# Optimization experiments

Hardware: AMD Instinct MI355X
Metric: run time of the kernel (lower is better)

The kernel has to match this reference:

```python
import jax, jax.numpy as jnp
import numpy as np

B, L, C = 8, 2048, 512
CI = C // 2  # internal_units


def setup_inputs() -> dict:
    key = jax.random.key(0)
    ks = jax.random.split(key, 4)
    inputs = jax.random.normal(ks[0], (B, L, C), dtype=jnp.float32)
    # Conv1D kernel_size=1 == per-position linear; kernel_initializer='random_normal' (stddev 0.05)
    Wx = 0.05 * jax.random.normal(ks[1], (C, CI), dtype=jnp.float32)
    Wy = 0.05 * jax.random.normal(ks[2], (C, CI), dtype=jnp.float32)
    Wo = 0.05 * jax.random.normal(ks[3], (C, C), dtype=jnp.float32)
    bx = jnp.zeros((CI,), dtype=jnp.float32)
    by = jnp.zeros((CI,), dtype=jnp.float32)
    bo = jnp.zeros((C,), dtype=jnp.float32)
    return {"inputs": inputs, "Wx": Wx, "bx": bx, "Wy": Wy, "by": by, "Wo": Wo, "bo": bo}


def reference(inputs, Wx, bx, Wy, by, Wo, bo):
    # 1x1 conv projections (per-position linear layers with bias)
    x_proj = jnp.einsum('blc,ci->bli', inputs, Wx) + bx   # [B, L, Ci]
    y_proj = jnp.einsum('blc,ci->bli', inputs, Wy) + by   # [B, L, Ci]
    o_proj = jnp.einsum('blc,cd->bld', inputs, Wo) + bo   # [B, L, C]
    # scores: batched matmul x @ y^T -> [B, L, L]
    scores = jnp.einsum('bli,bmi->blm', x_proj, y_proj)
    # NOTE: softmax over axis=0 (the BATCH axis), as in the original module
    attn = jax.nn.softmax(scores, axis=0)
    s_dot = jnp.einsum('blm,bmc->blc', attn, o_proj)       # [B, L, C]
    return inputs + s_dot
```

## Files before the change

kernel.cpp:

```cpp
#include <hip/hip_runtime.h>


#define NB 8
#define NL 2048
#define NC 512
#define NCI 256

using f16x8 = __attribute__((ext_vector_type(8))) _Float16;
using f32x4 = __attribute__((ext_vector_type(4))) float;
typedef unsigned short u16;

__device__ __forceinline__ u16 f16b(float x) {
    _Float16 h = (_Float16)x;
    return __builtin_bit_cast(u16, h);
}
__device__ __forceinline__ float f16tof(u16 u) {
    return (float)__builtin_bit_cast(_Float16, u);
}
__device__ __forceinline__ void gload16(const void* g, void* l) {
    __builtin_amdgcn_global_load_lds((__attribute__((address_space(1))) void*)g,
                                     (__attribute__((address_space(3))) void*)l,
                                     16, 0, 0);
}

__global__ __launch_bounds__(256) void cvt_x_kernel(const float* __restrict__ X,
                                                    u16* __restrict__ Xf)
{
    size_t i = (size_t)blockIdx.x * 256 + threadIdx.x;
    const float4* X4 = (const float4*)X;
    float4 a = X4[2 * i], b = X4[2 * i + 1];
    u16 o[8] = {f16b(a.x), f16b(a.y), f16b(a.z), f16b(a.w),
                f16b(b.x), f16b(b.y), f16b(b.z), f16b(b.w)};
    ((uint4*)Xf)[i] = *(const uint4*)o;
}

__global__ __launch_bounds__(256) void cvt_w_kernel(
    const float* __restrict__ Wx, const float* __restrict__ Wy, const float* __restrict__ Wo,
    u16* __restrict__ WxT, u16* __restrict__ WyT, u16* __restrict__ WoT)
{
    const int bid = blockIdx.x, t = threadIdx.x;
#pragma unroll
    for (int kk = 0; kk < 2; ++kk) {
        const int k = t + kk * 256;
        if (bid < 256)      WxT[(size_t)bid * NC + k] = f16b(Wx[(size_t)k * NCI + bid]);
        else if (bid < 512) WyT[(size_t)(bid - 256) * NC + k] = f16b(Wy[(size_t)k * NCI + (bid - 256)]);
        else                WoT[(size_t)(bid - 512) * NC + k] = f16b(Wo[(size_t)k * NC + (bid - 512)]);
    }
}

__global__ __launch_bounds__(256) void proj_kernel(
    const u16* __restrict__ Xf,
    const u16* __restrict__ WxT, const u16* __restrict__ WyT, const u16* __restrict__ WoT,
    const float* __restrict__ bx, const float* __restrict__ by, const float* __restrict__ bo,
    u16* __restrict__ xp, u16* __restrict__ yp, u16* __restrict__ opT)
{
    __shared__ __align__(16) u16 SM[17408];
    u16* As = SM;
    u16* Bs = SM + 8192;

    const int tid = threadIdx.x;
    const int w = tid >> 6, lane = tid & 63;
    const int row0 = blockIdx.x * 128;
    const int cb = blockIdx.y;

    const u16* W; const float* bias; int n0, path;
    if (cb < 2)      { path = 0; n0 = cb * 128;       W = WxT; bias = bx; }
    else if (cb < 4) { path = 1; n0 = (cb - 2) * 128; W = WyT; bias = by; }
    else             { path = 2; n0 = (cb - 4) * 128; W = WoT; bias = bo; }

    f32x4 acc[4][4] = {};
    const int wm = (w & 1) * 64, wn = (w >> 1) * 64;
    const int fr = lane & 15, fq = lane >> 4;

    for (int k0 = 0; k0 < NC; k0 += 64) {
#pragma unroll
        for (int pass = 0; pass < 4; ++pass) {
            const int cbase = pass * 256 + w * 64;
            const int chunk = cbase + lane;
            const int r = chunk >> 3;
            const int kc = (chunk & 7) ^ (r & 7);
            gload16(Xf + (size_t)(row0 + r) * NC + k0 + kc * 8, (char*)As + cbase * 16);
            gload16(W  + (size_t)(n0  + r) * NC + k0 + kc * 8, (char*)Bs + cbase * 16);
        }
        __syncthreads();
        f16x8 a[4][2], b[4][2];
#pragma unroll
        for (int mi = 0; mi < 4; ++mi)
#pragma unroll
            for (int kt = 0; kt < 2; ++kt)
                a[mi][kt] = *(const f16x8*)&As[(wm + mi * 16 + fr) * 64 + ((kt * 4 + fq) ^ (fr & 7)) * 8];
#pragma unroll
        for (int ni = 0; ni < 4; ++ni)
#pragma unroll
            for (int kt = 0; kt < 2; ++kt)
                b[ni][kt] = *(const f16x8*)&Bs[(wn + ni * 16 + fr) * 64 + ((kt * 4 + fq) ^ (fr & 7)) * 8];
#pragma unroll
        for (int kt = 0; kt < 2; ++kt)
#pragma unroll
            for (int mi = 0; mi < 4; ++mi)
#pragma unroll
                for (int ni = 0; ni < 4; ++ni)
                    acc[mi][ni] = __builtin_amdgcn_mfma_f32_16x16x32_f16(a[mi][kt], b[ni][kt], acc[mi][ni], 0, 0, 0);
        __syncthreads();
    }

    if (path != 2) {
        u16* O = (path == 0) ? xp : yp;
#pragma unroll
        for (int mi = 0; mi < 4; ++mi) {
            const int grow = row0 + wm + mi * 16 + fq * 4;
#pragma unroll
            for (int ni = 0; ni < 4; ++ni) {
                const int gcol = n0 + wn + ni * 16 + fr;
                const float bv = bias[gcol];
#pragma unroll
                for (int r = 0; r < 4; ++r)
                    O[(size_t)(grow + r) * NCI + gcol] = f16b(acc[mi][ni][r] + bv);
            }
        }
    } else {
        u16* Ts = SM;
#pragma unroll
        for (int mi = 0; mi < 4; ++mi) {
            const int mb = wm + mi * 16 + fq * 4;
#pragma unroll
            for (int ni = 0; ni < 4; ++ni) {
                const int nl_ = wn + ni * 16 + fr;
                const float bv = bias[n0 + nl_];
#pragma unroll
                for (int r = 0; r < 4; ++r)
                    Ts[nl_ * 136 + mb + r] = f16b(acc[mi][ni][r] + bv);
            }
        }
        __syncthreads();
        const int b = row0 >> 11, m0 = row0 & 2047;
        u16* dst = opT + (size_t)b * NC * NL + (size_t)n0 * NL + m0;
        for (int i = tid; i < 128 * 16; i += 256) {
            const int c = i >> 4, ch = i & 15;
            uint4 v = *(const uint4*)&Ts[c * 136 + ch * 8];
            *(uint4*)&dst[(size_t)c * NL + ch * 8] = v;
        }
    }
}

__global__ __launch_bounds__(512, 4) void score_softmax_kernel(
    const u16* __restrict__ xp, const u16* __restrict__ yp, u16* __restrict__ ATT)
{
    __shared__ __align__(16) u16 SM[33280];
    const int tid = threadIdx.x;
    const int w = tid >> 6, lane = tid & 63;

    const int L = blockIdx.x + 32 * blockIdx.y;
    const int xcd = L & 7, slot = L >> 3;
    const int bx = (xcd >> 1) * 8 + (slot & 7);
    const int by = (xcd & 1) * 16 + (slot >> 3);
    const int row0 = bx * 64, col0 = by * 64;

    const int bb = w & 3, nh = w >> 2;
    const int fr = lane & 15, fq = lane >> 4;

    const int rs = (tid >> 3) & 63;
    const int jj = (tid & 7) ^ (rs & 7);

    unsigned sv[2][16];

#pragma unroll
    for (int g = 0; g < 2; ++g) {
        f32x4 acc[4][2] = {};
#pragma unroll
        for (int s = 0; s < 4; ++s) {
            const int k0 = s * 64;
#pragma unroll
            for (int pass = 0; pass < 8; ++pass) {
                const int ab = pass >> 2, b2 = pass & 3;
                const u16* src = (ab ? yp : xp)
                    + (size_t)(g * 4 + b2) * NL * NCI
                    + (size_t)((ab ? col0 : row0) + rs) * NCI + k0 + jj * 8;
                gload16(src, (char*)SM + pass * 8192 + tid * 16);
            }
            __syncthreads();
#pragma unroll
            for (int kt = 0; kt < 2; ++kt) {
                const int coff = ((kt * 4 + fq) ^ (fr & 7)) * 8;
                f16x8 af[4], bf[2];
#pragma unroll
                for (int mi = 0; mi < 4; ++mi)
                    af[mi] = *(const f16x8*)&SM[bb * 4096 + (mi * 16 + fr) * 64 + coff];
#pragma unroll
                for (int ni = 0; ni < 2; ++ni)
                    bf[ni] = *(const f16x8*)&SM[16384 + bb * 4096 + (nh * 32 + ni * 16 + fr) * 64 + coff];
#pragma unroll
                for (int mi = 0; mi < 4; ++mi)
#pragma unroll
                    for (int ni = 0; ni < 2; ++ni)
                        acc[mi][ni] = __builtin_amdgcn_mfma_f32_16x16x32_f16(af[mi], bf[ni], acc[mi][ni], 0, 0, 0);
            }
            __syncthreads();
        }
#pragma unroll
        for (int mi = 0; mi < 4; ++mi)
#pragma unroll
            for (int ni = 0; ni < 2; ++ni) {
                sv[g][mi * 4 + ni * 2 + 0] = (unsigned)f16b(acc[mi][ni][0]) | ((unsigned)f16b(acc[mi][ni][1]) << 16);
                sv[g][mi * 4 + ni * 2 + 1] = (unsigned)f16b(acc[mi][ni][2]) | ((unsigned)f16b(acc[mi][ni][3]) << 16);
            }
    }

#pragma unroll
    for (int g = 0; g < 2; ++g)
#pragma unroll
        for (int mi = 0; mi < 4; ++mi)
#pragma unroll
            for (int ni = 0; ni < 2; ++ni)
#pragma unroll
                for (int rp = 0; rp < 2; ++rp) {
                    const unsigned u = sv[g][mi * 4 + ni * 2 + rp];
                    const int r_ = mi * 16 + fq * 4 + rp * 2;
                    const int c_ = nh * 32 + ni * 16 + fr;
                    SM[(r_ * 65 + c_) * 8 + g * 4 + bb]         = (u16)(u & 0xFFFF);
                    SM[((r_ + 1) * 65 + c_) * 8 + g * 4 + bb]   = (u16)(u >> 16);
                }
    __syncthreads();

#pragma unroll
    for (int j = 0; j < 8; ++j) {
        const int row = j * 8 + w;
        const int col = lane;
        const uint4 v = *(const uint4*)&SM[(row * 65 + col) * 8];
        float f[NB];
        f[0] = f16tof((u16)(v.x & 0xFFFF)); f[1] = f16tof((u16)(v.x >> 16));
        f[2] = f16tof((u16)(v.y & 0xFFFF)); f[3] = f16tof((u16)(v.y >> 16));
        f[4] = f16tof((u16)(v.z & 0xFFFF)); f[5] = f16tof((u16)(v.z >> 16));
        f[6] = f16tof((u16)(v.w & 0xFFFF)); f[7] = f16tof((u16)(v.w >> 16));
        float m = f[0];
#pragma unroll
        for (int b = 1; b < NB; ++b) m = fmaxf(m, f[b]);
        float ssum = 0.f;
#pragma unroll
        for (int b = 0; b < NB; ++b) { f[b] = __expf(f[b] - m); ssum += f[b]; }
        const float inv = 1.f / ssum;
        const size_t go = (size_t)(row0 + row) * NL + col0 + col;
#pragma unroll
        for (int b = 0; b < NB; ++b)
            ATT[(size_t)b * NL * NL + go] = f16b(f[b] * inv);
    }
}

__global__ __launch_bounds__(512) void out_kernel(
    const u16* __restrict__ ATT, const u16* __restrict__ opT,
    const float* __restrict__ X, float* __restrict__ Out)
{
    __shared__ __align__(16) u16 As[16384], Bs[16384];
    const int tid = threadIdx.x;
    const int w = tid >> 6, lane = tid & 63;

    const int id  = blockIdx.x + 16 * (blockIdx.y + 4 * blockIdx.z);
    const int nid = (id & 7) * 64 + (id >> 3);
    const int bx  = nid & 15;
    const int by  = (nid >> 4) & 3;
    const int b   = nid >> 6;

    const int row0 = bx * 128, col0 = by * 128;
    const u16* Aatt = ATT + (size_t)b * NL * NL;
    const u16* Bsrc = opT + (size_t)b * NC * NL;

    f32x4 acc[4][2] = {};
    const int wm = (w & 1) * 64, wn = (w >> 1) * 32;
    const int fr = lane & 15, fq = lane >> 4;

    for (int it = 0; it < NL / 128; ++it) {
        const int k0 = it * 128;
#pragma unroll
        for (int pass = 0; pass < 4; ++pass) {
            const int c = pass * 512 + tid;
            const int kh = c >> 10;
            const int r = (c >> 3) & 127;
            const int jj = (c & 7) ^ (r & 7);
            const int srck = k0 + kh * 64 + jj * 8;
            gload16(Aatt + (size_t)(row0 + r) * NL + srck, (char*)As + c * 16);
            gload16(Bsrc + (size_t)(col0 + r) * NL + srck, (char*)Bs + c * 16);
        }
        __syncthreads();
#pragma unroll
        for (int kh = 0; kh < 2; ++kh)
#pragma unroll
            for (int kt = 0; kt < 2; ++kt) {
                const int hb = kh * 8192;
                const int coff = ((kt * 4 + fq) ^ (fr & 7)) * 8;
                f16x8 af[4], bf[2];
#pragma unroll
                for (int mi = 0; mi < 4; ++mi)
                    af[mi] = *(const f16x8*)&As[hb + (wm + mi * 16 + fr) * 64 + coff];
#pragma unroll
                for (int ni = 0; ni < 2; ++ni)
                    bf[ni] = *(const f16x8*)&Bs[hb + (wn + ni * 16 + fr) * 64 + coff];
#pragma unroll
                for (int mi = 0; mi < 4; ++mi)
#pragma unroll
                    for (int ni = 0; ni < 2; ++ni)
                        acc[mi][ni] = __builtin_amdgcn_mfma_f32_16x16x32_f16(af[mi], bf[ni], acc[mi][ni], 0, 0, 0);
            }
        __syncthreads();
    }
    const size_t ob = (size_t)b * NL * NC;
#pragma unroll
    for (int mi = 0; mi < 4; ++mi) {
        const int gr = row0 + wm + mi * 16 + fq * 4;
#pragma unroll
        for (int ni = 0; ni < 2; ++ni) {
            const int gc = col0 + wn + ni * 16 + fr;
#pragma unroll
            for (int r = 0; r < 4; ++r) {
                const size_t o = ob + (size_t)(gr + r) * NC + gc;
                Out[o] = X[o] + acc[mi][ni][r];
            }
        }
    }
}

extern "C" void kernel_launch(void* const* d_in, const int* in_sizes, int n_in,
                              void* d_out, int out_size, void* d_ws, size_t ws_size,
                              hipStream_t stream)
{
    const float* X  = (const float*)d_in[0];
    const float* Wx = (const float*)d_in[1];
    const float* bx = (const float*)d_in[2];
    const float* Wy = (const float*)d_in[3];
    const float* by = (const float*)d_in[4];
    const float* Wo = (const float*)d_in[5];
    const float* bo = (const float*)d_in[6];
    float* out = (float*)d_out;

    char* ws = (char*)d_ws;
    u16* ATT = (u16*)ws;
    u16* Xf  = (u16*)ws;
    char* p = ws + 67108864;
    u16* xp  = (u16*)p; p += 8388608;
    u16* yp  = (u16*)p; p += 8388608;
    u16* opT = (u16*)p; p += 16777216;
    u16* WxT = (u16*)p; p += 262144;
    u16* WyT = (u16*)p; p += 262144;
    u16* WoT = (u16*)p; p += 524288;

    cvt_x_kernel<<<4096, 256, 0, stream>>>(X, Xf);
    cvt_w_kernel<<<1024, 256, 0, stream>>>(Wx, Wy, Wo, WxT, WyT, WoT);
    proj_kernel<<<dim3(128, 8), 256, 0, stream>>>(Xf, WxT, WyT, WoT, bx, by, bo, xp, yp, opT);
    score_softmax_kernel<<<dim3(32, 32), 512, 0, stream>>>(xp, yp, ATT);
    out_kernel<<<dim3(16, 4, NB), 512, 0, stream>>>(ATT, opT, X, out);
}
```

Measured before the change: 203.6 us.

## Fuse fp32-to-fp16 input conversion into projection and coalesce attention stores via LDS

Removes the separate cvt_x kernel: proj_kernel now loads fp32 input directly, converts to fp16 in registers and writes the swizzled tile to LDS, saving one launch and a 16MB round trip. In score_softmax_kernel, softmax outputs are staged per batch in LDS and written back as 16-byte vectors instead of scattered 2-byte stores. The trade-off is that proj_kernel reads twice the input bytes per tile through synchronous register loads instead of async global-to-LDS loads, and the score kernel uses more LDS and adds barriers, which may lower occupancy.

New measurement: 207.7 us. +2.1%, slower.

```diff
diff --git a/kernel.cpp b/kernel.cpp
--- a/kernel.cpp
+++ b/kernel.cpp
@@ -21,17 +21,6 @@
     __builtin_amdgcn_global_load_lds((__attribute__((address_space(1))) void*)g,
                                      (__attribute__((address_space(3))) void*)l,
                                      16, 0, 0);
-}
-
-__global__ __launch_bounds__(256) void cvt_x_kernel(const float* __restrict__ X,
-                                                    u16* __restrict__ Xf)
-{
-    size_t i = (size_t)blockIdx.x * 256 + threadIdx.x;
-    const float4* X4 = (const float4*)X;
-    float4 a = X4[2 * i], b = X4[2 * i + 1];
-    u16 o[8] = {f16b(a.x), f16b(a.y), f16b(a.z), f16b(a.w),
-                f16b(b.x), f16b(b.y), f16b(b.z), f16b(b.w)};
-    ((uint4*)Xf)[i] = *(const uint4*)o;
 }
 
 __global__ __launch_bounds__(256) void cvt_w_kernel(
@@ -49,7 +38,7 @@
 }
 
 __global__ __launch_bounds__(256) void proj_kernel(
-    const u16* __restrict__ Xf,
+    const float* __restrict__ X,
     const u16* __restrict__ WxT, const u16* __restrict__ WyT, const u16* __restrict__ WoT,
     const float* __restrict__ bx, const float* __restrict__ by, const float* __restrict__ bo,
     u16* __restrict__ xp, u16* __restrict__ yp, u16* __restrict__ opT)
@@ -79,8 +68,12 @@
             const int chunk = cbase + lane;
             const int r = chunk >> 3;
             const int kc = (chunk & 7) ^ (r & 7);
-            gload16(Xf + (size_t)(row0 + r) * NC + k0 + kc * 8, (char*)As + cbase * 16);
-            gload16(W  + (size_t)(n0  + r) * NC + k0 + kc * 8, (char*)Bs + cbase * 16);
+            const float* xs = X + (size_t)(row0 + r) * NC + k0 + kc * 8;
+            const float4 lo = *(const float4*)xs, hi = *(const float4*)(xs + 4);
+            u16 o[8] = {f16b(lo.x), f16b(lo.y), f16b(lo.z), f16b(lo.w),
+                        f16b(hi.x), f16b(hi.y), f16b(hi.z), f16b(hi.w)};
+            *(uint4*)&As[chunk * 8] = *(const uint4*)o;
+            gload16(W + (size_t)(n0 + r) * NC + k0 + kc * 8, (char*)Bs + cbase * 16);
         }
         __syncthreads();
         f16x8 a[4][2], b[4][2];
@@ -146,7 +139,7 @@
 __global__ __launch_bounds__(512, 4) void score_softmax_kernel(
     const u16* __restrict__ xp, const u16* __restrict__ yp, u16* __restrict__ ATT)
 {
-    __shared__ __align__(16) u16 SM[33280];
+    __shared__ __align__(16) u16 SM[36864];
     const int tid = threadIdx.x;
     const int w = tid >> 6, lane = tid & 63;
 
@@ -222,11 +215,18 @@
                 }
     __syncthreads();
 
+    uint4 v8[8];
 #pragma unroll
     for (int j = 0; j < 8; ++j) {
         const int row = j * 8 + w;
-        const int col = lane;
-        const uint4 v = *(const uint4*)&SM[(row * 65 + col) * 8];
+        v8[j] = *(const uint4*)&SM[(row * 65 + lane) * 8];
+    }
+    __syncthreads();
+
+#pragma unroll
+    for (int j = 0; j < 8; ++j) {
+        const int row = j * 8 + w;
+        const uint4 v = v8[j];
         float f[NB];
         f[0] = f16tof((u16)(v.x & 0xFFFF)); f[1] = f16tof((u16)(v.x >> 16));
         f[2] = f16tof((u16)(v.y & 0xFFFF)); f[3] = f16tof((u16)(v.y >> 16));
@@ -239,10 +239,19 @@
 #pragma unroll
         for (int b = 0; b < NB; ++b) { f[b] = __expf(f[b] - m); ssum += f[b]; }
         const float inv = 1.f / ssum;
-        const size_t go = (size_t)(row0 + row) * NL + col0 + col;
 #pragma unroll
         for (int b = 0; b < NB; ++b)
-            ATT[(size_t)b * NL * NL + go] = f16b(f[b] * inv);
+            SM[b * 4608 + row * 72 + lane] = f16b(f[b] * inv);
+    }
+    __syncthreads();
+
+#pragma unroll
+    for (int i = 0; i < 8; ++i) {
+        const int q = i * 512 + tid;
+        const int b = q >> 9, rem = q & 511;
+        const int row = rem >> 3, cg = rem & 7;
+        const uint4 val = *(const uint4*)&SM[b * 4608 + row * 72 + cg * 8];
+        *(uint4*)&ATT[(size_t)b * NL * NL + (size_t)(row0 + row) * NL + col0 + cg * 8] = val;
     }
 }
 
@@ -333,7 +342,6 @@
 
     char* ws = (char*)d_ws;
     u16* ATT = (u16*)ws;
-    u16* Xf  = (u16*)ws;
     char* p = ws + 67108864;
     u16* xp  = (u16*)p; p += 8388608;
     u16* yp  = (u16*)p; p += 8388608;
@@ -342,9 +350,8 @@
     u16* WyT = (u16*)p; p += 262144;
     u16* WoT = (u16*)p; p += 524288;
 
-    cvt_x_kernel<<<4096, 256, 0, stream>>>(X, Xf);
     cvt_w_kernel<<<1024, 256, 0, stream>>>(Wx, Wy, Wo, WxT, WyT, WoT);
-    proj_kernel<<<dim3(128, 8), 256, 0, stream>>>(Xf, WxT, WyT, WoT, bx, by, bo, xp, yp, opT);
+    proj_kernel<<<dim3(128, 8), 256, 0, stream>>>(X, WxT, WyT, WoT, bx, by, bo, xp, yp, opT);
     score_softmax_kernel<<<dim3(32, 32), 512, 0, stream>>>(xp, yp, ATT);
     out_kernel<<<dim3(16, 4, NB), 512, 0, stream>>>(ATT, opT, X, out);
 }
```
